# Performance work log

Measured on AMD Instinct MI355X. Metric: run time of the kernel, lower is better.

Reference implementation:

```python
import jax, jax.numpy as jnp
import numpy as np
from jax import lax

BN_EPS = 1e-5


def setup_inputs() -> dict:
    key = jax.random.key(0)
    k = jax.random.split(key, 7)
    B, H, W = 128, 224, 224
    return {
        "x": jax.random.normal(k[0], (B, 1, H, W), dtype=jnp.float32),
        "conv_w": jax.random.normal(k[1], (16, 1, 5, 5), dtype=jnp.float32) * 0.1,
        "conv_b": jax.random.normal(k[2], (16,), dtype=jnp.float32) * 0.1,
        "gamma": jax.random.uniform(k[3], (16,), dtype=jnp.float32, minval=0.5, maxval=1.5),
        "beta": jax.random.normal(k[4], (16,), dtype=jnp.float32) * 0.1,
        "run_mean": jax.random.normal(k[5], (16,), dtype=jnp.float32) * 0.1,
        "run_var": jax.random.uniform(k[6], (16,), dtype=jnp.float32, minval=0.5, maxval=1.5),
    }


def reference(x, conv_w, conv_b, gamma, beta, run_mean, run_var):
    # Conv2d(1,16,5,stride=1,padding=2): NCHW x OIHW -> NCHW
    y = lax.conv_general_dilated(
        x, conv_w, window_strides=(1, 1), padding=[(2, 2), (2, 2)],
        dimension_numbers=("NCHW", "OIHW", "NCHW"))
    y = y + conv_b[None, :, None, None]
    # BatchNorm2d(16) in inference form with running stats
    scale = gamma * lax.rsqrt(run_var + BN_EPS)
    y = y * scale[None, :, None, None] + (beta - run_mean * scale)[None, :, None, None]
    # ReLU
    y = jnp.maximum(y, 0.0)
    # MaxPool2d(kernel=2, stride=2)
    out = lax.reduce_window(y, -jnp.inf, lax.max,
                            window_dimensions=(1, 1, 2, 2),
                            window_strides=(1, 1, 2, 2),
                            padding="VALID")
    return out  # [B, 16, H/2, W/2]
```

## Files before the change

### kernel.cpp

```cpp
#include <hip/hip_runtime.h>
#include <stdint.h>

#define IMG 224
#define OUT_DIM 112
#define NCH 16
#define TILE_Y 32
#define R_ROWS 36
#define HJ 116
#define HSZ (R_ROWS * HJ)

typedef _Float16 h8t  __attribute__((ext_vector_type(8)));
typedef float    f32x4 __attribute__((ext_vector_type(4)));
typedef uint32_t u32x4 __attribute__((ext_vector_type(4)));

__global__ __launch_bounds__(256)
void conv_bn_relu_pool(const float* __restrict__ x,
                       const float* __restrict__ conv_w,
                       const float* __restrict__ conv_b,
                       const float* __restrict__ gamma,
                       const float* __restrict__ beta,
                       const float* __restrict__ run_mean,
                       const float* __restrict__ run_var,
                       float* __restrict__ out)
{
    __shared__ __align__(16) uint32_t H[2 * HSZ];

    const int tid = threadIdx.x;
    const int b   = blockIdx.y;
    const int ty  = blockIdx.x * TILE_Y;
    const float* xb = x + (size_t)b * IMG * IMG;

    const int lane = tid & 63;
    const int wv   = tid >> 6;
    const int pp   = lane & 15;
    const int g    = lane >> 4;

    const float* w = conv_w + pp * 25;
    float w0 = w[g*5+0], w1 = w[g*5+1], w2 = w[g*5+2], w3 = w[g*5+3], w4 = w[g*5+4];
    float e0 = (2*g   < 5) ? w[20 + 2*g]     : 0.f;
    float e1 = (2*g+1 < 5) ? w[20 + 2*g + 1] : 0.f;
    u32x4 bu;
    bu[0] = __builtin_bit_cast(uint32_t, __builtin_amdgcn_cvt_pkrtz(w0, w1));
    bu[1] = __builtin_bit_cast(uint32_t, __builtin_amdgcn_cvt_pkrtz(w2, w3));
    bu[2] = __builtin_bit_cast(uint32_t, __builtin_amdgcn_cvt_pkrtz(w4, 0.f));
    bu[3] = __builtin_bit_cast(uint32_t, __builtin_amdgcn_cvt_pkrtz(e0, e1));
    h8t B1 = __builtin_bit_cast(h8t, bu);
    float sc = gamma[pp] * rsqrtf(run_var[pp] + 1e-5f);
    float sh = fmaf(sc, conv_b[pp] - run_mean[pp], beta[pp]);

    for (int i = tid; i < R_ROWS * 56; i += 256) {
        int r = i / 56, q = i - r * 56;
        int gy = ty - 2 + r;
        int c  = 4 * q;
        f32x4 v = {0.f, 0.f, 0.f, 0.f};
        float v4 = 0.f;
        if ((unsigned)gy < IMG) {
            const float* row = xb + gy * IMG;
            v = *(const f32x4*)(row + c);
            if (q < 55) v4 = row[c + 4];
        }
        uint32_t* base = H + r * HJ + 2 + (c >> 1);
        uint2 p0, p1;
        p0.x = __builtin_bit_cast(uint32_t, __builtin_amdgcn_cvt_pkrtz(v[0], v[1]));
        p0.y = __builtin_bit_cast(uint32_t, __builtin_amdgcn_cvt_pkrtz(v[2], v[3]));
        p1.x = __builtin_bit_cast(uint32_t, __builtin_amdgcn_cvt_pkrtz(v[1], v[2]));
        p1.y = __builtin_bit_cast(uint32_t, __builtin_amdgcn_cvt_pkrtz(v[3], v4));
        *(uint2*)(base)       = p0;
        *(uint2*)(base + HSZ) = p1;
    }
    if (tid < 2 * R_ROWS) {
        int pl = tid & 1, r = tid >> 1;
        int gy = ty - 2 + r;
        float f0 = 0.f;
        if (pl == 1 && (unsigned)gy < IMG) f0 = xb[gy * IMG];
        uint32_t pm1 = __builtin_bit_cast(uint32_t, __builtin_amdgcn_cvt_pkrtz(0.f, f0));
        uint32_t* row = H + pl * HSZ + r * HJ;
        row[0] = 0u;
        row[1] = pl ? pm1 : 0u;
        *(uint2*)(row + 114) = make_uint2(0u, 0u);
    }
    __syncthreads();

    const uint32_t* Hq = H + (pp & 1) * HSZ + (pp >> 1) + 1;
    float* outb = out + ((size_t)b * NCH + pp) * (OUT_DIM * OUT_DIM);

    #pragma unroll
    for (int s = 0; s < 4; ++s) {
        const int y0 = 8 * wv + 2 * s;
        const int oy = blockIdx.x * 16 + 4 * wv + s;
        const uint32_t* rA = Hq + (y0 + g) * HJ;
        const uint32_t* r4 = Hq + (y0 + 4) * HJ + g;
        float* orow = outb + oy * OUT_DIM + 2 * g;

        #pragma unroll
        for (int sub = 0; sub < 14; ++sub) {
            const int j0 = sub * 8;
            f32x4 accA = {0.f, 0.f, 0.f, 0.f};
            f32x4 accB = {0.f, 0.f, 0.f, 0.f};

            u32x4 a1 = { rA[j0], rA[j0 + 1], rA[j0 + 2], r4[j0] };
            accA = __builtin_amdgcn_mfma_f32_16x16x32_f16(
                       __builtin_bit_cast(h8t, a1), B1, accA, 0, 0, 0);
            u32x4 c1 = { rA[j0 + HJ], rA[j0 + 1 + HJ], rA[j0 + 2 + HJ], r4[j0 + HJ] };
            accB = __builtin_amdgcn_mfma_f32_16x16x32_f16(
                       __builtin_bit_cast(h8t, c1), B1, accB, 0, 0, 0);

            float m0 = fmaxf(fmaxf(accA[0], accA[1]), fmaxf(accB[0], accB[1]));
            float m1 = fmaxf(fmaxf(accA[2], accA[3]), fmaxf(accB[2], accB[3]));
            float y0v = fmaxf(fmaf(m0, sc, sh), 0.f);
            float y1v = fmaxf(fmaf(m1, sc, sh), 0.f);
            *(float2*)(orow + sub * 8) = make_float2(y0v, y1v);
        }
    }
}

extern "C" void kernel_launch(void* const* d_in, const int* in_sizes, int n_in,
                              void* d_out, int out_size, void* d_ws, size_t ws_size,
                              hipStream_t stream) {
    const float* x        = (const float*)d_in[0];
    const float* conv_w   = (const float*)d_in[1];
    const float* conv_b   = (const float*)d_in[2];
    const float* gamma    = (const float*)d_in[3];
    const float* beta     = (const float*)d_in[4];
    const float* run_mean = (const float*)d_in[5];
    const float* run_var  = (const float*)d_in[6];
    float* out = (float*)d_out;

    dim3 grid(IMG / TILE_Y, 128);
    dim3 block(256);
    conv_bn_relu_pool<<<grid, block, 0, stream>>>(
        x, conv_w, conv_b, gamma, beta, run_mean, run_var, out);
}
```

Baseline: 148.1 us.

## Split tile staging into two halves, prefetching the second during first-half compute

The input halo load is split. Only the first 20 rows are staged into LDS before the first sync. The remaining rows are issued as global loads into registers before the first half of the MFMA compute runs, then converted and written to LDS after it, followed by a second barrier. This is meant to hide global load latency behind compute in the single-block-per-tile design. It costs extra registers for the prefetch buffers and adds a second __syncthreads. Rows are regrouped so each wave handles two output rows per half.

```diff
diff --git a/kernel.cpp b/kernel.cpp
--- a/kernel.cpp
+++ b/kernel.cpp
@@ -6,8 +6,12 @@
 #define NCH 16
 #define TILE_Y 32
 #define R_ROWS 36
+#define A_ROWS 20
 #define HJ 116
 #define HSZ (R_ROWS * HJ)
+#define QW 56
+#define A_ITEMS (A_ROWS * QW)
+#define T_ITEMS (R_ROWS * QW)
 
 typedef _Float16 h8t  __attribute__((ext_vector_type(8)));
 typedef float    f32x4 __attribute__((ext_vector_type(4)));
@@ -48,8 +52,8 @@
     float sc = gamma[pp] * rsqrtf(run_var[pp] + 1e-5f);
     float sh = fmaf(sc, conv_b[pp] - run_mean[pp], beta[pp]);
 
-    for (int i = tid; i < R_ROWS * 56; i += 256) {
-        int r = i / 56, q = i - r * 56;
+    for (int i = tid; i < A_ITEMS; i += 256) {
+        int r = i / QW, q = i - r * QW;
         int gy = ty - 2 + r;
         int c  = 4 * q;
         f32x4 v = {0.f, 0.f, 0.f, 0.f};
@@ -57,7 +61,7 @@
         if ((unsigned)gy < IMG) {
             const float* row = xb + gy * IMG;
             v = *(const f32x4*)(row + c);
-            if (q < 55) v4 = row[c + 4];
+            if (q < QW - 1) v4 = row[c + 4];
         }
         uint32_t* base = H + r * HJ + 2 + (c >> 1);
         uint2 p0, p1;
@@ -81,37 +85,80 @@
     }
     __syncthreads();
 
+    f32x4 pv[4];
+    float pw[4];
+    #pragma unroll
+    for (int k = 0; k < 4; ++k) {
+        int i = A_ITEMS + tid + 256 * k;
+        pv[k] = (f32x4){0.f, 0.f, 0.f, 0.f};
+        pw[k] = 0.f;
+        if (i < T_ITEMS) {
+            int r = i / QW, q = i - r * QW;
+            int gy = ty - 2 + r;
+            int c  = 4 * q;
+            if ((unsigned)gy < IMG) {
+                const float* row = xb + gy * IMG;
+                pv[k] = *(const f32x4*)(row + c);
+                if (q < QW - 1) pw[k] = row[c + 4];
+            }
+        }
+    }
+
     const uint32_t* Hq = H + (pp & 1) * HSZ + (pp >> 1) + 1;
     float* outb = out + ((size_t)b * NCH + pp) * (OUT_DIM * OUT_DIM);
 
+    auto compute_half = [&](int h) {
+        #pragma unroll
+        for (int s = 0; s < 2; ++s) {
+            const int y0 = 16 * h + 4 * wv + 2 * s;
+            const int oy = blockIdx.x * 16 + 8 * h + 2 * wv + s;
+            const uint32_t* rA = Hq + (y0 + g) * HJ;
+            const uint32_t* r4 = Hq + (y0 + 4) * HJ + g;
+            float* orow = outb + oy * OUT_DIM + 2 * g;
+
+            #pragma unroll
+            for (int sub = 0; sub < 14; ++sub) {
+                const int j0 = sub * 8;
+                f32x4 accA = {0.f, 0.f, 0.f, 0.f};
+                f32x4 accB = {0.f, 0.f, 0.f, 0.f};
+
+                u32x4 a1 = { rA[j0], rA[j0 + 1], rA[j0 + 2], r4[j0] };
+                accA = __builtin_amdgcn_mfma_f32_16x16x32_f16(
+                           __builtin_bit_cast(h8t, a1), B1, accA, 0, 0, 0);
+                u32x4 c1 = { rA[j0 + HJ], rA[j0 + 1 + HJ], rA[j0 + 2 + HJ], r4[j0 + HJ] };
+                accB = __builtin_amdgcn_mfma_f32_16x16x32_f16(
+                           __builtin_bit_cast(h8t, c1), B1, accB, 0, 0, 0);
+
+                float m0 = fmaxf(fmaxf(accA[0], accA[1]), fmaxf(accB[0], accB[1]));
+                float m1 = fmaxf(fmaxf(accA[2], accA[3]), fmaxf(accB[2], accB[3]));
+                float y0v = fmaxf(fmaf(m0, sc, sh), 0.f);
+                float y1v = fmaxf(fmaf(m1, sc, sh), 0.f);
+                *(float2*)(orow + sub * 8) = make_float2(y0v, y1v);
+            }
+        }
+    };
+
+    compute_half(0);
+
     #pragma unroll
-    for (int s = 0; s < 4; ++s) {
-        const int y0 = 8 * wv + 2 * s;
-        const int oy = blockIdx.x * 16 + 4 * wv + s;
-        const uint32_t* rA = Hq + (y0 + g) * HJ;
-        const uint32_t* r4 = Hq + (y0 + 4) * HJ + g;
-        float* orow = outb + oy * OUT_DIM + 2 * g;
-
-        #pragma unroll
-        for (int sub = 0; sub < 14; ++sub) {
-            const int j0 = sub * 8;
-            f32x4 accA = {0.f, 0.f, 0.f, 0.f};
-            f32x4 accB = {0.f, 0.f, 0.f, 0.f};
-
-            u32x4 a1 = { rA[j0], rA[j0 + 1], rA[j0 + 2], r4[j0] };
-            accA = __builtin_amdgcn_mfma_f32_16x16x32_f16(
-                       __builtin_bit_cast(h8t, a1), B1, accA, 0, 0, 0);
-            u32x4 c1 = { rA[j0 + HJ], rA[j0 + 1 + HJ], rA[j0 + 2 + HJ], r4[j0 + HJ] };
-            accB = __builtin_amdgcn_mfma_f32_16x16x32_f16(
-                       __builtin_bit_cast(h8t, c1), B1, accB, 0, 0, 0);
-
-            float m0 = fmaxf(fmaxf(accA[0], accA[1]), fmaxf(accB[0], accB[1]));
-            float m1 = fmaxf(fmaxf(accA[2], accA[3]), fmaxf(accB[2], accB[3]));
-            float y0v = fmaxf(fmaf(m0, sc, sh), 0.f);
-            float y1v = fmaxf(fmaf(m1, sc, sh), 0.f);
-            *(float2*)(orow + sub * 8) = make_float2(y0v, y1v);
+    for (int k = 0; k < 4; ++k) {
+        int i = A_ITEMS + tid + 256 * k;
+        if (i < T_ITEMS) {
+            int r = i / QW, q = i - r * QW;
+            int c = 4 * q;
+            uint32_t* base = H + r * HJ + 2 + (c >> 1);
+            uint2 p0, p1;
+            p0.x = __builtin_bit_cast(uint32_t, __builtin_amdgcn_cvt_pkrtz(pv[k][0], pv[k][1]));
+            p0.y = __builtin_bit_cast(uint32_t, __builtin_amdgcn_cvt_pkrtz(pv[k][2], pv[k][3]));
+            p1.x = __builtin_bit_cast(uint32_t, __builtin_amdgcn_cvt_pkrtz(pv[k][1], pv[k][2]));
+            p1.y = __builtin_bit_cast(uint32_t, __builtin_amdgcn_cvt_pkrtz(pv[k][3], pw[k]));
+            *(uint2*)(base)       = p0;
+            *(uint2*)(base + HSZ) = p1;
         }
     }
+    __syncthreads();
+
+    compute_half(1);
 }
 
 extern "C" void kernel_launch(void* const* d_in, const int* in_sizes, int n_in,
```

Result: slower. 156.8 us (+5.8%).
